# Optimization experiments

Measured on AMD Instinct MI355X. Metric: run time of the kernel, lower is better.

The kernel has to match this reference:

```python
import jax, jax.numpy as jnp
import numpy as np

H = 32   # num_heads
G = 8    # num_groups (KV heads)
GS = H // G  # group_size
D_MODEL = 2048
HEAD_DIM = D_MODEL // H  # 64


def setup_inputs() -> dict:
    key = jax.random.key(0)
    ks = jax.random.split(key, 9)
    B, S = 2, 2048
    s_in = 1.0 / np.sqrt(D_MODEL)
    return {
        "x": jax.random.normal(ks[0], (B, S, D_MODEL), jnp.float32),
        "Wq": jax.random.normal(ks[1], (D_MODEL, H * HEAD_DIM), jnp.float32) * s_in,
        "bq": jnp.zeros((H * HEAD_DIM,), jnp.float32),
        "Wk": jax.random.normal(ks[2], (D_MODEL, G * HEAD_DIM), jnp.float32) * s_in,
        "bk": jnp.zeros((G * HEAD_DIM,), jnp.float32),
        "Wv": jax.random.normal(ks[3], (D_MODEL, G * HEAD_DIM), jnp.float32) * s_in,
        "bv": jnp.zeros((G * HEAD_DIM,), jnp.float32),
        "Wo": jax.random.normal(ks[4], (H * HEAD_DIM, D_MODEL), jnp.float32) * s_in,
        "bo": jnp.zeros((D_MODEL,), jnp.float32),
    }


def reference(x, Wq, bq, Wk, bk, Wv, bv, Wo, bo):
    B, S, _ = x.shape
    scale = 1.0 / np.sqrt(HEAD_DIM)
    # Projections
    q = (x @ Wq + bq).reshape(B, S, H, HEAD_DIM)          # [B,S,H,D]
    k = (x @ Wk + bk).reshape(B, S, G, HEAD_DIM)          # [B,S,G,D]
    v = (x @ Wv + bv).reshape(B, S, G, HEAD_DIM)
    # Group heads: head h belongs to group h // GS (matches repeat_interleave)
    q = q.reshape(B, S, G, GS, HEAD_DIM).transpose(0, 2, 3, 1, 4)  # [B,G,GS,S,D]
    k = k.transpose(0, 2, 1, 3)                                    # [B,G,S,D]
    v = v.transpose(0, 2, 1, 3)                                    # [B,G,S,D]
    # scores[b,g,m,s,t] = q[b,g,m,s,:] . k[b,g,t,:]
    scores = jnp.einsum('bgmsd,bgtd->bgmst', q, k) * scale
    attn = jax.nn.softmax(scores, axis=-1)
    ctx = jnp.einsum('bgmst,bgtd->bgmsd', attn, v)                 # [B,G,GS,S,D]
    ctx = ctx.transpose(0, 3, 1, 2, 4).reshape(B, S, H * HEAD_DIM)  # [B,S,d_model]
    return ctx @ Wo + bo
```

## Files before the change

kernel.cpp:

```cpp
#include <hip/hip_runtime.h>
#include <stdint.h>

#define DEVINL __device__ __forceinline__

typedef unsigned short u16;
typedef unsigned int   u32;
typedef __attribute__((ext_vector_type(8)))  __bf16 bf16x8;
typedef __attribute__((ext_vector_type(4)))  float  f32x4;
typedef __attribute__((ext_vector_type(16))) float  f32x16;
typedef __attribute__((ext_vector_type(4)))  u32    u32x4;

static constexpr int SEQ    = 2048;
static constexpr int DMODEL = 2048;
static constexpr int NHEAD  = 32;
static constexpr int NGRP   = 8;
static constexpr int DHEAD  = 64;
static constexpr int MTOK   = 2 * SEQ;
static constexpr int NQKV   = NHEAD*DHEAD + 2*NGRP*DHEAD;

DEVINL u16 f2bf(float f) {
  unsigned u = __builtin_bit_cast(unsigned, f);
  u += 0x7fffu + ((u >> 16) & 1u);
  return (u16)(u >> 16);
}

DEVINL void gld16(const void* g, void* l) {
  typedef __attribute__((address_space(1))) const void* gp_t;
  typedef __attribute__((address_space(3))) void* lp_t;
  __builtin_amdgcn_global_load_lds((gp_t)g, (lp_t)l, 16, 0, 0);
}

DEVINL f32x4 mfma16(bf16x8 a, bf16x8 b, f32x4 c) {
  return __builtin_amdgcn_mfma_f32_16x16x32_bf16(a, b, c, 0, 0, 0);
}
DEVINL f32x16 mfma32(bf16x8 a, bf16x8 b, f32x16 c) {
  return __builtin_amdgcn_mfma_f32_32x32x16_bf16(a, b, c, 0, 0, 0);
}
DEVINL u32 cvtpk(float lo, float hi_) {
  u32 r;
  asm("v_cvt_pk_bf16_f32 %0, %1, %2" : "=v"(r) : "v"(lo), "v"(hi_));
  return r;
}
DEVINL void plswap(u32& a, u32& b) {
  asm("v_permlane32_swap_b32 %0, %1" : "+v"(a), "+v"(b));
}

__global__ void k_cvt(const float* __restrict__ s, u16* __restrict__ d) {
  int i = (blockIdx.x * 256 + threadIdx.x) * 4;
  float4 v = *reinterpret_cast<const float4*>(s + i);
  ushort4 o;
  o.x = f2bf(v.x); o.y = f2bf(v.y); o.z = f2bf(v.z); o.w = f2bf(v.w);
  *reinterpret_cast<ushort4*>(d + i) = o;
}

__global__ void k_tconv(const float* __restrict__ src, u16* __restrict__ dst, int N) {
  __shared__ float t[32][33];
  int n0 = blockIdx.x * 32, k0 = blockIdx.y * 32;
  int tx = threadIdx.x, ty = threadIdx.y;
  #pragma unroll
  for (int r = 0; r < 32; r += 8)
    t[r + ty][tx] = src[(size_t)(k0 + r + ty) * N + n0 + tx];
  __syncthreads();
  #pragma unroll
  for (int r = 0; r < 32; r += 8)
    dst[(size_t)(n0 + r + ty) * DMODEL + k0 + tx] = f2bf(t[tx][r + ty]);
}

__global__ void k_packbias(const float* __restrict__ bq, const float* __restrict__ bk,
                           const float* __restrict__ bv, float* __restrict__ d) {
  int i = blockIdx.x * 256 + threadIdx.x;
  d[i] = i < 2048 ? bq[i] : (i < 2560 ? bk[i - 2048] : bv[i - 2560]);
}

template<int ISV>
__global__ void k_pack(const u16* __restrict__ qkv, u16* __restrict__ out) {
  __shared__ u16 t[64][72];
  const int blk = blockIdx.x;
  const int sblk = blk & 31, g = (blk >> 5) & 7, bb = blk >> 8;
  const int tid = threadIdx.x;
  const size_t srcbase = ((size_t)bb * SEQ + sblk * 64) * NQKV + (ISV ? 2560 : 2048) + g * 64;
  #pragma unroll
  for (int i = 0; i < 2; ++i) {
    int c = tid * 2 + i;
    int row = c >> 3, dc = (c & 7) * 8;
    *(bf16x8*)&t[row][dc] = *(const bf16x8*)(qkv + srcbase + (size_t)row * NQKV + dc);
  }
  __syncthreads();
  const int bg = bb * 8 + g;
  #pragma unroll
  for (int r = 0; r < 2; ++r) {
    int f = tid + 256 * r;
    int lane = f & 63, cj = (f >> 6) & 3, stl = f >> 8;
    int q = lane & 31, hi = lane >> 5;
    size_t o = ((((size_t)bg * 64 + sblk * 2 + stl) * 4 + cj) * 64 + lane) * 8;
    if (ISV) {
      int dcol = (cj & 1) * 32 + q;
      int s0 = stl * 32 + (cj >> 1) * 16 + hi * 8;
      u16 tmp[8];
      #pragma unroll
      for (int e = 0; e < 8; ++e) tmp[e] = t[s0 + e][dcol];
      *(ushort4*)(out + o)     = *(ushort4*)&tmp[0];
      *(ushort4*)(out + o + 4) = *(ushort4*)&tmp[4];
    } else {
      int srow = stl * 32 + q;
      int d0 = cj * 16 + hi * 8;
      *(bf16x8*)(out + o) = *(const bf16x8*)&t[srow][d0];
    }
  }
}

template<int F32OUT>
__global__ __launch_bounds__(256, 3)
void k_gemm(const u16* __restrict__ A, const u16* __restrict__ Bt,
            const float* __restrict__ bias, void* __restrict__ Cv,
            int K, int ldc)
{
  __shared__ __align__(16) u16 lA[128 * 32];
  __shared__ __align__(16) u16 lB[128 * 32];
  const int tid = threadIdx.x;
  const int lane = tid & 63, wid = tid >> 6;
  const int fr = lane & 15, fq = lane >> 4;
  const int n0 = blockIdx.x * 128, m0 = blockIdx.y * 128;
  const int wr = wid >> 1, wc = wid & 1;

  f32x4 acc[4][4];
  #pragma unroll
  for (int i = 0; i < 4; ++i)
    #pragma unroll
    for (int j = 0; j < 4; ++j) acc[i][j] = f32x4{0.f, 0.f, 0.f, 0.f};

  const int s0 = (wid * 2 + 0) * 64 + lane;
  const int s1 = (wid * 2 + 1) * 64 + lane;
  const int r0 = s0 >> 2, k0s = 8 * (s0 & 3);
  const int r1 = s1 >> 2, k1s = 8 * (s1 & 3);
  const u16* gA0 = A  + (size_t)(m0 + r0) * K + k0s;
  const u16* gA1 = A  + (size_t)(m0 + r1) * K + k1s;
  const u16* gB0 = Bt + (size_t)(n0 + r0) * K + k0s;
  const u16* gB1 = Bt + (size_t)(n0 + r1) * K + k1s;
  u16* lA0 = &lA[(wid * 2 + 0) * 512];
  u16* lA1 = &lA[(wid * 2 + 1) * 512];
  u16* lB0 = &lB[(wid * 2 + 0) * 512];
  u16* lB1 = &lB[(wid * 2 + 1) * 512];

  int aoff[4], boff[4];
  #pragma unroll
  for (int i = 0; i < 4; ++i) {
    aoff[i] = (wr * 64 + i * 16 + fr) * 64 + fq * 16;
    boff[i] = (wc * 64 + i * 16 + fr) * 64 + fq * 16;
  }
  const char* laB = (const char*)lA;
  const char* lbB = (const char*)lB;

  for (int kt = 0; kt < K; kt += 32) {
    gld16(gA0, lA0); gld16(gA1, lA1);
    gld16(gB0, lB0); gld16(gB1, lB1);
    gA0 += 32; gA1 += 32; gB0 += 32; gB1 += 32;
    __syncthreads();
    bf16x8 a[4], b[4];
    #pragma unroll
    for (int i = 0; i < 4; ++i) a[i] = *(const bf16x8*)(laB + aoff[i]);
    #pragma unroll
    for (int j = 0; j < 4; ++j) b[j] = *(const bf16x8*)(lbB + boff[j]);
    #pragma unroll
    for (int i = 0; i < 4; ++i)
      #pragma unroll
      for (int j = 0; j < 4; ++j)
        acc[i][j] = mfma16(a[i], b[j], acc[i][j]);
    __syncthreads();
  }

  #pragma unroll
  for (int i = 0; i < 4; ++i) {
    const int row = m0 + wr * 64 + i * 16 + fq * 4;
    #pragma unroll
    for (int j = 0; j < 4; ++j) {
      const int col = n0 + wc * 64 + j * 16 + fr;
      const float bvl = bias[col];
      #pragma unroll
      for (int t = 0; t < 4; ++t) {
        const float val = acc[i][j][t] + bvl;
        if (F32OUT)
          ((float*)Cv)[(size_t)(row + t) * ldc + col] = val;
        else
          ((u16*)Cv)[(size_t)(row + t) * ldc + col] = f2bf(val);
      }
    }
  }
}

__global__ __launch_bounds__(256, 4)
void k_attn(const u16* __restrict__ qkv, const u16* __restrict__ kswz,
            const u16* __restrict__ vswz, u16* __restrict__ ctx)
{
  __shared__ float lm[2][64], ll[2][64];
  __shared__ float lo[2][32][64];
  const int tid = threadIdx.x, lane = tid & 63, wid = tid >> 6;
  const int q = lane & 31, hi = lane >> 5;
  const int qg = wid >> 1, kvh = wid & 1;
  const int h = blockIdx.y, bb = blockIdx.z, g = h >> 2;
  const int qrow = blockIdx.x * 64 + qg * 32 + q;
  const size_t tokbase = (size_t)bb * SEQ;

  bf16x8 aq[4];
  {
    const u16* qp = qkv + (tokbase + qrow) * NQKV + h * 64 + hi * 8;
    #pragma unroll
    for (int c = 0; c < 4; ++c) aq[c] = *(const bf16x8*)(qp + 16 * c);
  }
  f32x16 o0, o1;
  #pragma unroll
  for (int r = 0; r < 16; ++r) { o0[r] = 0.f; o1[r] = 0.f; }
  float m = -3e38f, l = 0.f;

  const int bg = bb * 8 + g;
  const u16* kb = kswz + (size_t)bg * 131072 + lane * 8;
  const u16* vb = vswz + (size_t)bg * 131072 + lane * 8;

  const float cs  = 0.18033688011112042f;
  const float thr = 44.3614195558365f;

  const int st0 = kvh * 32, st1 = st0 + 32;

  bf16x8 kf[4];
  #pragma unroll
  for (int c = 0; c < 4; ++c) kf[c] = *(const bf16x8*)(kb + (st0 * 4 + c) * 512);

  for (int st = st0; st < st1; ++st) {
    bf16x8 vf[4];
    #pragma unroll
    for (int j = 0; j < 4; ++j) vf[j] = *(const bf16x8*)(vb + (st * 4 + j) * 512);

    f32x16 s;
    #pragma unroll
    for (int r = 0; r < 16; ++r) s[r] = 0.f;
    __builtin_amdgcn_s_setprio(1);
    #pragma unroll
    for (int c = 0; c < 4; ++c) s = mfma32(kf[c], aq[c], s);
    __builtin_amdgcn_s_setprio(0);

    {
      const int sn = (st + 1 < SEQ / 32) ? st + 1 : st;
      #pragma unroll
      for (int c = 0; c < 4; ++c) kf[c] = *(const bf16x8*)(kb + (sn * 4 + c) * 512);
    }

    float m1 = fmaxf(fmaxf(s[0],  s[1]),  s[2]);
    float m2 = fmaxf(fmaxf(s[3],  s[4]),  s[5]);
    float m3 = fmaxf(fmaxf(s[6],  s[7]),  s[8]);
    float m4 = fmaxf(fmaxf(s[9],  s[10]), s[11]);
    float m5 = fmaxf(fmaxf(s[12], s[13]), s[14]);
    float mx = fmaxf(fmaxf(fmaxf(fmaxf(m1, m2), m3), fmaxf(m4, m5)), s[15]);
    mx = fmaxf(mx, __shfl_xor(mx, 32));

    if (!__all(mx - m <= thr)) {
      const float mn = fmaxf(m, mx);
      const float rs = exp2f((m - mn) * cs);
      m = mn; l *= rs;
      #pragma unroll
      for (int r = 0; r < 16; ++r) { o0[r] *= rs; o1[r] *= rs; }
    }

    const float mb = m * cs;
    float p[16];
    #pragma unroll
    for (int r = 0; r < 16; ++r) p[r] = exp2f(s[r] * cs - mb);
    float a8[8];
    #pragma unroll
    for (int r = 0; r < 8; ++r) a8[r] = p[r] + p[r + 8];
    float sum = ((a8[0] + a8[4]) + (a8[1] + a8[5])) + ((a8[2] + a8[6]) + (a8[3] + a8[7]));
    sum += __shfl_xor(sum, 32);
    l += sum;

    u32 w0 = cvtpk(p[0],  p[1]),  w1 = cvtpk(p[2],  p[3]);
    u32 w2 = cvtpk(p[4],  p[5]),  w3 = cvtpk(p[6],  p[7]);
    u32 w4 = cvtpk(p[8],  p[9]),  w5 = cvtpk(p[10], p[11]);
    u32 w6 = cvtpk(p[12], p[13]), w7 = cvtpk(p[14], p[15]);

    plswap(w0, w2);  plswap(w1, w3);
    plswap(w4, w6);  plswap(w5, w7);
    u32x4 t0, t1;
    t0.x = w0; t0.y = w1; t0.z = w2; t0.w = w3;
    t1.x = w4; t1.y = w5; t1.z = w6; t1.w = w7;
    bf16x8 pb0 = __builtin_bit_cast(bf16x8, t0);
    bf16x8 pb1 = __builtin_bit_cast(bf16x8, t1);

    __builtin_amdgcn_s_setprio(1);
    o0 = mfma32(vf[0], pb0, o0);
    o1 = mfma32(vf[1], pb0, o1);
    o0 = mfma32(vf[2], pb1, o0);
    o1 = mfma32(vf[3], pb1, o1);
    __builtin_amdgcn_s_setprio(0);
  }

  if (kvh == 1) {
    lm[qg][lane] = m;
    ll[qg][lane] = l;
    #pragma unroll
    for (int r = 0; r < 16; ++r) {
      lo[qg][r][lane]      = o0[r];
      lo[qg][16 + r][lane] = o1[r];
    }
  }
  __syncthreads();
  if (kvh == 0) {
    const float mp = lm[qg][lane], lp = ll[qg][lane];
    const float mn = fmaxf(m, mp);
    const float w1 = exp2f((m - mn) * cs);
    const float w2 = exp2f((mp - mn) * cs);
    const float inv = 1.0f / (l * w1 + lp * w2);
    u16* cp = ctx + (tokbase + qrow) * DMODEL + h * 64;
    #pragma unroll
    for (int t = 0; t < 4; ++t) {
      ushort4 oa, ob;
      oa.x = f2bf((o0[4*t+0] * w1 + lo[qg][4*t+0][lane] * w2) * inv);
      oa.y = f2bf((o0[4*t+1] * w1 + lo[qg][4*t+1][lane] * w2) * inv);
      oa.z = f2bf((o0[4*t+2] * w1 + lo[qg][4*t+2][lane] * w2) * inv);
      oa.w = f2bf((o0[4*t+3] * w1 + lo[qg][4*t+3][lane] * w2) * inv);
      *reinterpret_cast<ushort4*>(cp + 8*t + 4*hi) = oa;
      ob.x = f2bf((o1[4*t+0] * w1 + lo[qg][16+4*t+0][lane] * w2) * inv);
      ob.y = f2bf((o1[4*t+1] * w1 + lo[qg][16+4*t+1][lane] * w2) * inv);
      ob.z = f2bf((o1[4*t+2] * w1 + lo[qg][16+4*t+2][lane] * w2) * inv);
      ob.w = f2bf((o1[4*t+3] * w1 + lo[qg][16+4*t+3][lane] * w2) * inv);
      *reinterpret_cast<ushort4*>(cp + 32 + 8*t + 4*hi) = ob;
    }
  }
}

extern "C" void kernel_launch(void* const* d_in, const int* in_sizes, int n_in,
                              void* d_out, int out_size, void* d_ws, size_t ws_size,
                              hipStream_t stream) {
  const float* x  = (const float*)d_in[0];
  const float* Wq = (const float*)d_in[1];
  const float* bq = (const float*)d_in[2];
  const float* Wk = (const float*)d_in[3];
  const float* bk = (const float*)d_in[4];
  const float* Wv = (const float*)d_in[5];
  const float* bv = (const float*)d_in[6];
  const float* Wo = (const float*)d_in[7];
  const float* bo = (const float*)d_in[8];

  char* ws = (char*)d_ws;
  size_t off = 0;
  auto take = [&](size_t bytes) { char* p = ws + off; off += (bytes + 255) & ~(size_t)255; return p; };
  u16*   xb    = (u16*)  take((size_t)MTOK * DMODEL * 2);
  u16*   wqkvT = (u16*)  take((size_t)NQKV * DMODEL * 2);
  u16*   woT   = (u16*)  take((size_t)DMODEL * DMODEL * 2);
  u16*   qkv   = (u16*)  take((size_t)MTOK * NQKV * 2);
  u16*   kswz  = (u16*)  take((size_t)16 * 131072 * 2);
  u16*   vswz  = (u16*)  take((size_t)16 * 131072 * 2);
  float* bqkv  = (float*)take((size_t)NQKV * 4);

  if (off > ws_size) {
    hipMemsetAsync(d_out, 0, (size_t)out_size * 4, stream);
    return;
  }

  dim3 tb(32, 8);
  k_cvt<<<(MTOK * DMODEL) / (4 * 256), 256, 0, stream>>>(x, xb);
  k_tconv<<<dim3(64, 64), tb, 0, stream>>>(Wq, wqkvT, 2048);
  k_tconv<<<dim3(16, 64), tb, 0, stream>>>(Wk, wqkvT + (size_t)2048 * DMODEL, 512);
  k_tconv<<<dim3(16, 64), tb, 0, stream>>>(Wv, wqkvT + (size_t)2560 * DMODEL, 512);
  k_tconv<<<dim3(64, 64), tb, 0, stream>>>(Wo, woT, 2048);
  k_packbias<<<NQKV / 256, 256, 0, stream>>>(bq, bk, bv, bqkv);

  k_gemm<0><<<dim3(NQKV / 128, MTOK / 128), 256, 0, stream>>>(
      xb, wqkvT, bqkv, qkv, DMODEL, NQKV);

  k_pack<0><<<512, 256, 0, stream>>>(qkv, kswz);
  k_pack<1><<<512, 256, 0, stream>>>(qkv, vswz);

  u16* ctxb = xb;
  k_attn<<<dim3(SEQ / 64, NHEAD, 2), 256, 0, stream>>>(qkv, kswz, vswz, ctxb);

  k_gemm<1><<<dim3(DMODEL / 128, MTOK / 128), 256, 0, stream>>>(
      ctxb, woT, bo, d_out, DMODEL, DMODEL);
}
```

Before: 259.6 us.

## Stage K/V tiles through double-buffered LDS with async global-to-LDS loads

```diff
diff --git a/kernel.cpp b/kernel.cpp
--- a/kernel.cpp
+++ b/kernel.cpp
@@ -192,14 +192,14 @@
 void k_attn(const u16* __restrict__ qkv, const u16* __restrict__ kswz,
             const u16* __restrict__ vswz, u16* __restrict__ ctx)
 {
-  __shared__ float lm[2][64], ll[2][64];
-  __shared__ float lo[2][32][64];
+  __shared__ __align__(16) u16 sbuf[16384];
   const int tid = threadIdx.x, lane = tid & 63, wid = tid >> 6;
   const int q = lane & 31, hi = lane >> 5;
   const int qg = wid >> 1, kvh = wid & 1;
   const int h = blockIdx.y, bb = blockIdx.z, g = h >> 2;
   const int qrow = blockIdx.x * 64 + qg * 32 + q;
   const size_t tokbase = (size_t)bb * SEQ;
+  const int bg = bb * 8 + g;
 
   bf16x8 aq[4];
   {
@@ -212,23 +212,32 @@
   for (int r = 0; r < 16; ++r) { o0[r] = 0.f; o1[r] = 0.f; }
   float m = -3e38f, l = 0.f;
 
-  const int bg = bb * 8 + g;
-  const u16* kb = kswz + (size_t)bg * 131072 + lane * 8;
-  const u16* vb = vswz + (size_t)bg * 131072 + lane * 8;
+  const int skvh  = wid >> 1;
+  const int fbase = (wid & 1) * 4;
+  const u16* sb = ((wid & 1) ? vswz : kswz) + (size_t)bg * 131072 + lane * 8;
 
   const float cs  = 0.18033688011112042f;
   const float thr = 44.3614195558365f;
 
-  const int st0 = kvh * 32, st1 = st0 + 32;
-
-  bf16x8 kf[4];
-  #pragma unroll
-  for (int c = 0; c < 4; ++c) kf[c] = *(const bf16x8*)(kb + (st0 * 4 + c) * 512);
-
-  for (int st = st0; st < st1; ++st) {
-    bf16x8 vf[4];
-    #pragma unroll
-    for (int j = 0; j < 4; ++j) vf[j] = *(const bf16x8*)(vb + (st * 4 + j) * 512);
+  #pragma unroll
+  for (int e = 0; e < 4; ++e)
+    gld16(sb + (size_t)((skvh * 32) * 4 + e) * 512,
+          &sbuf[skvh * 4096 + (fbase + e) * 512]);
+  __syncthreads();
+
+  int buf = 0;
+  for (int i = 0; i < 32; ++i) {
+    if (i + 1 < 32) {
+      #pragma unroll
+      for (int e = 0; e < 4; ++e)
+        gld16(sb + (size_t)((skvh * 32 + i + 1) * 4 + e) * 512,
+              &sbuf[(buf ^ 1) * 8192 + skvh * 4096 + (fbase + e) * 512]);
+    }
+    const u16* cb = &sbuf[buf * 8192 + kvh * 4096];
+
+    bf16x8 kf[4];
+    #pragma unroll
+    for (int c = 0; c < 4; ++c) kf[c] = *(const bf16x8*)(cb + c * 512 + lane * 8);
 
     f32x16 s;
     #pragma unroll
@@ -238,11 +247,9 @@
     for (int c = 0; c < 4; ++c) s = mfma32(kf[c], aq[c], s);
     __builtin_amdgcn_s_setprio(0);
 
-    {
-      const int sn = (st + 1 < SEQ / 32) ? st + 1 : st;
-      #pragma unroll
-      for (int c = 0; c < 4; ++c) kf[c] = *(const bf16x8*)(kb + (sn * 4 + c) * 512);
-    }
+    bf16x8 vf[4];
+    #pragma unroll
+    for (int j = 0; j < 4; ++j) vf[j] = *(const bf16x8*)(cb + (4 + j) * 512 + lane * 8);
 
     float m1 = fmaxf(fmaxf(s[0],  s[1]),  s[2]);
     float m2 = fmaxf(fmaxf(s[3],  s[4]),  s[5]);
@@ -275,7 +282,6 @@
     u32 w2 = cvtpk(p[4],  p[5]),  w3 = cvtpk(p[6],  p[7]);
     u32 w4 = cvtpk(p[8],  p[9]),  w5 = cvtpk(p[10], p[11]);
     u32 w6 = cvtpk(p[12], p[13]), w7 = cvtpk(p[14], p[15]);
-
     plswap(w0, w2);  plswap(w1, w3);
     plswap(w4, w6);  plswap(w5, w7);
     u32x4 t0, t1;
@@ -290,37 +296,42 @@
     o0 = mfma32(vf[2], pb1, o0);
     o1 = mfma32(vf[3], pb1, o1);
     __builtin_amdgcn_s_setprio(0);
-  }
-
+
+    __syncthreads();
+    buf ^= 1;
+  }
+
+  float* lmf = (float*)sbuf;
   if (kvh == 1) {
-    lm[qg][lane] = m;
-    ll[qg][lane] = l;
+    lmf[qg * 64 + lane] = m;
+    lmf[128 + qg * 64 + lane] = l;
     #pragma unroll
     for (int r = 0; r < 16; ++r) {
-      lo[qg][r][lane]      = o0[r];
-      lo[qg][16 + r][lane] = o1[r];
+      lmf[256 + (qg * 32 + r) * 64 + lane]      = o0[r];
+      lmf[256 + (qg * 32 + 16 + r) * 64 + lane] = o1[r];
     }
   }
   __syncthreads();
   if (kvh == 0) {
-    const float mp = lm[qg][lane], lp = ll[qg][lane];
+    const float mp = lmf[qg * 64 + lane], lp = lmf[128 + qg * 64 + lane];
     const float mn = fmaxf(m, mp);
     const float w1 = exp2f((m - mn) * cs);
     const float w2 = exp2f((mp - mn) * cs);
     const float inv = 1.0f / (l * w1 + lp * w2);
+    const float* lop = &lmf[256 + qg * 32 * 64 + lane];
     u16* cp = ctx + (tokbase + qrow) * DMODEL + h * 64;
     #pragma unroll
     for (int t = 0; t < 4; ++t) {
       ushort4 oa, ob;
-      oa.x = f2bf((o0[4*t+0] * w1 + lo[qg][4*t+0][lane] * w2) * inv);
-      oa.y = f2bf((o0[4*t+1] * w1 + lo[qg][4*t+1][lane] * w2) * inv);
-      oa.z = f2bf((o0[4*t+2] * w1 + lo[qg][4*t+2][lane] * w2) * inv);
-      oa.w = f2bf((o0[4*t+3] * w1 + lo[qg][4*t+3][lane] * w2) * inv);
+      oa.x = f2bf((o0[4*t+0] * w1 + lop[(4*t+0) * 64] * w2) * inv);
+      oa.y = f2bf((o0[4*t+1] * w1 + lop[(4*t+1) * 64] * w2) * inv);
+      oa.z = f2bf((o0[4*t+2] * w1 + lop[(4*t+2) * 64] * w2) * inv);
+      oa.w = f2bf((o0[4*t+3] * w1 + lop[(4*t+3) * 64] * w2) * inv);
       *reinterpret_cast<ushort4*>(cp + 8*t + 4*hi) = oa;
-      ob.x = f2bf((o1[4*t+0] * w1 + lo[qg][16+4*t+0][lane] * w2) * inv);
-      ob.y = f2bf((o1[4*t+1] * w1 + lo[qg][16+4*t+1][lane] * w2) * inv);
-      ob.z = f2bf((o1[4*t+2] * w1 + lo[qg][16+4*t+2][lane] * w2) * inv);
-      ob.w = f2bf((o1[4*t+3] * w1 + lo[qg][16+4*t+3][lane] * w2) * inv);
+      ob.x = f2bf((o1[4*t+0] * w1 + lop[(16+4*t+0) * 64] * w2) * inv);
+      ob.y = f2bf((o1[4*t+1] * w1 + lop[(16+4*t+1) * 64] * w2) * inv);
+      ob.z = f2bf((o1[4*t+2] * w1 + lop[(16+4*t+2) * 64] * w2) * inv);
+      ob.w = f2bf((o1[4*t+3] * w1 + lop[(16+4*t+3) * 64] * w2) * inv);
       *reinterpret_cast<ushort4*>(cp + 32 + 8*t + 4*hi) = ob;
     }
   }
```

New measurement: 260.0 us. Within noise of the previous version (+0.2%).
